# Performance work log

Hardware: AMD Instinct MI355X
Metric: run time of the kernel (lower is better)

## Reference

```python
import jax, jax.numpy as jnp
import numpy as np

NSTEP, NGRID = 365, 50000
PRECS = 1e-05
# [lo, hi] physical ranges for the first 12 HBV parameters (routing params unused, routOpt=False)
PARA_RANGES = np.array([
    [1, 6], [50, 1000], [0.05, 0.9], [0.01, 0.5], [0.001, 0.2], [0.2, 1],
    [0, 10], [0, 100], [-2.5, 2.5], [0.5, 10], [0, 0.1], [0, 0.2],
], dtype=np.float32)


def setup_inputs() -> dict:
    key = jax.random.key(0)
    k1, k2 = jax.random.split(key)
    x = jax.random.uniform(k1, (NSTEP, NGRID, 3), dtype=jnp.float32)
    parameters = jax.random.uniform(k2, (NGRID, 14), dtype=jnp.float32)
    return {"x": x, "parameters": parameters}


def _hbv_forward(x, parameters):
    P = x[:, :, 0]       # precip   [Nstep, Ngrid]
    T = x[:, :, 1]       # temp
    ETpot = x[:, :, 2]   # potential ET
    lo = jnp.asarray(PARA_RANGES[:, 0])
    hi = jnp.asarray(PARA_RANGES[:, 1])
    p = lo + parameters[:, :12] * (hi - lo)  # [Ngrid, 12]
    (parBETA, parFC, parK0, parK1, parK2, parLP, parPERC, parUZL,
     parTT, parCFMAX, parCFR, parCWH) = [p[:, i] for i in range(12)]

    ngrid = P.shape[1]
    init = tuple(jnp.full((ngrid,), 0.001, dtype=jnp.float32) for _ in range(5))

    def step(carry, inp):
        SNOWPACK, MELTWATER, SM, SUZ, SLZ = carry
        PRECIP, Tt, ETp = inp
        is_rain = (Tt >= parTT).astype(jnp.float32)
        RAIN = PRECIP * is_rain
        SNOW = PRECIP * (1.0 - is_rain)
        SNOWPACK = SNOWPACK + SNOW
        melt = jnp.minimum(jnp.maximum(parCFMAX * (Tt - parTT), 0.0), SNOWPACK)
        MELTWATER = MELTWATER + melt
        SNOWPACK = SNOWPACK - melt
        refreezing = jnp.minimum(jnp.maximum(parCFR * parCFMAX * (parTT - Tt), 0.0), MELTWATER)
        SNOWPACK = SNOWPACK + refreezing
        MELTWATER = MELTWATER - refreezing
        tosoil = jnp.maximum(MELTWATER - parCWH * SNOWPACK, 0.0)
        MELTWATER = MELTWATER - tosoil
        soil_wetness = jnp.clip((SM / parFC) ** parBETA, 0.0, 1.0)
        recharge = (RAIN + tosoil) * soil_wetness
        SM = SM + RAIN + tosoil - recharge
        excess = jnp.maximum(SM - parFC, 0.0)
        SM = SM - excess
        evapfactor = jnp.clip(SM / (parLP * parFC), 0.0, 1.0)
        ETact = jnp.minimum(SM, ETp * evapfactor)
        SM = jnp.maximum(SM - ETact, PRECS)
        SUZ = SUZ + recharge + excess
        PERC = jnp.minimum(SUZ, parPERC)
        SUZ = SUZ - PERC
        Q0 = parK0 * jnp.maximum(SUZ - parUZL, 0.0)
        SUZ = SUZ - Q0
        Q1 = parK1 * SUZ
        SUZ = SUZ - Q1
        SLZ = SLZ + PERC
        Q2 = parK2 * SLZ
        SLZ = SLZ - Q2
        return (SNOWPACK, MELTWATER, SM, SUZ, SLZ), Q0 + Q1 + Q2

    _, Qsim = jax.lax.scan(step, init, (P, T, ETpot))
    return Qsim[..., None]  # [Nstep, Ngrid, 1]


def reference(x, parameters):
    return _hbv_forward(x, parameters)
```

## Files before the change

### kernel.cpp

```cpp
#include <hip/hip_runtime.h>

#define NSTEP 365
#define NGRID 50000
#define PRECS_F 1e-5f
#define CHUNK 16

#if defined(__has_builtin)
#  if __has_builtin(__builtin_amdgcn_exp2f) && __has_builtin(__builtin_amdgcn_logf)
#    define FAST_EXP2(x) __builtin_amdgcn_exp2f(x)
#    define FAST_LOG2(x) __builtin_amdgcn_logf(x)
#  endif
#endif
#ifndef FAST_EXP2
#  define FAST_EXP2(x) exp2f(x)
#  define FAST_LOG2(x) log2f(x)
#endif

__global__ __launch_bounds__(64) void hbv_kernel(const float* __restrict__ x,
                                                 const float* __restrict__ params,
                                                 float* __restrict__ out) {
    const int g = blockIdx.x * blockDim.x + threadIdx.x;
    if (g >= NGRID) return;

    const float* pr = params + (size_t)g * 14;
    float r0 = pr[0], r1 = pr[1], r2 = pr[2], r3 = pr[3], r4 = pr[4], r5 = pr[5];
    float r6 = pr[6], r7 = pr[7], r8 = pr[8], r9 = pr[9], r10 = pr[10], r11 = pr[11];

    const float parBETA  = 1.0f   + r0  * 5.0f;
    const float parFC    = 50.0f  + r1  * 950.0f;
    const float parK0    = 0.05f  + r2  * 0.85f;
    const float parK1    = 0.01f  + r3  * 0.49f;
    const float parK2    = 0.001f + r4  * 0.199f;
    const float parLP    = 0.2f   + r5  * 0.8f;
    const float parPERC  =          r6  * 10.0f;
    const float parUZL   =          r7  * 100.0f;
    const float parTT    = -2.5f  + r8  * 5.0f;
    const float parCFMAX = 0.5f   + r9  * 9.5f;
    const float parCFR   =          r10 * 0.1f;
    const float parCWH   =          r11 * 0.2f;

    const float invFC     = 1.0f / parFC;
    const float invLPFC   = 1.0f / (parLP * parFC);
    const float cfr_cfmax = parCFR * parCFMAX;

    float SNOWPACK = 0.001f, MELTWATER = 0.001f, SM = 0.001f, SUZ = 0.001f, SLZ = 0.001f;

    const int nchunks = (NSTEP + CHUNK - 1) / CHUNK;

    float AP[CHUNK], AT[CHUNK], AE[CHUNK];
    float BP[CHUNK], BT[CHUNK], BE[CHUNK];

    auto load_chunk = [&](int cidx, float (&P)[CHUNK], float (&T)[CHUNK], float (&E)[CHUNK]) {
        const int tbase = cidx * CHUNK;
        #pragma unroll
        for (int j = 0; j < CHUNK; ++j) {
            int t = tbase + j;
            t = (t < NSTEP) ? t : (NSTEP - 1);
            const float* p = x + ((size_t)t * NGRID + g) * 3;
            P[j] = p[0];
            T[j] = p[1];
            E[j] = p[2];
        }
    };

    auto compute_chunk = [&](int cidx, const float (&P)[CHUNK], const float (&T)[CHUNK],
                             const float (&E)[CHUNK]) {
        const int t0 = cidx * CHUNK;
        #pragma unroll
        for (int j = 0; j < CHUNK; ++j) {
            const float PRECIP = P[j];
            const float Tt     = T[j];
            const float ETp    = E[j];

            float RAIN = (Tt >= parTT) ? PRECIP : 0.0f;
            float SNOW = PRECIP - RAIN;
            SNOWPACK += SNOW;
            float melt = fminf(fmaxf(parCFMAX * (Tt - parTT), 0.0f), SNOWPACK);
            MELTWATER += melt;
            SNOWPACK  -= melt;
            float refreeze = fminf(fmaxf(cfr_cfmax * (parTT - Tt), 0.0f), MELTWATER);
            SNOWPACK  += refreeze;
            MELTWATER -= refreeze;
            float tosoil = fmaxf(MELTWATER - parCWH * SNOWPACK, 0.0f);
            MELTWATER -= tosoil;

            float ratio = SM * invFC;
            float sw = FAST_EXP2(parBETA * FAST_LOG2(ratio));
            sw = fminf(fmaxf(sw, 0.0f), 1.0f);
            float recharge = (RAIN + tosoil) * sw;
            SM += RAIN + tosoil - recharge;
            float excess = fmaxf(SM - parFC, 0.0f);
            SM -= excess;
            float evapfactor = fminf(fmaxf(SM * invLPFC, 0.0f), 1.0f);
            float ETact = fminf(SM, ETp * evapfactor);
            SM = fmaxf(SM - ETact, PRECS_F);

            SUZ += recharge + excess;
            float PERC = fminf(SUZ, parPERC);
            SUZ -= PERC;
            float Q0 = parK0 * fmaxf(SUZ - parUZL, 0.0f);
            SUZ -= Q0;
            float Q1 = parK1 * SUZ;
            SUZ -= Q1;
            SLZ += PERC;
            float Q2 = parK2 * SLZ;
            SLZ -= Q2;

            const int t = t0 + j;
            if (t < NSTEP) out[(size_t)t * NGRID + g] = Q0 + Q1 + Q2;
        }
    };

    load_chunk(0, AP, AT, AE);
    int c = 0;
    for (;;) {
        if (c + 1 < nchunks) load_chunk(c + 1, BP, BT, BE);
        compute_chunk(c, AP, AT, AE);
        if (++c >= nchunks) break;
        if (c + 1 < nchunks) load_chunk(c + 1, AP, AT, AE);
        compute_chunk(c, BP, BT, BE);
        if (++c >= nchunks) break;
    }
}

extern "C" void kernel_launch(void* const* d_in, const int* in_sizes, int n_in,
                              void* d_out, int out_size, void* d_ws, size_t ws_size,
                              hipStream_t stream) {
    const float* x      = (const float*)d_in[0];
    const float* params = (const float*)d_in[1];
    float* out          = (float*)d_out;

    const int block = 64;
    const int grid  = (NGRID + block - 1) / block;
    hbv_kernel<<<grid, block, 0, stream>>>(x, params, out);
}
```

Baseline: 324.3 us.

## Stage input chunks into LDS via async global_load_lds with double buffering

Replaces per-thread register prefetch of strided P/T/E values with coalesced 16-byte direct global-to-LDS loads covering each block's contiguous 192-float row segment per timestep, double-buffered across chunks. Explicit vmcnt waits let the next chunk's loads overlap computation of the current one. This aims to cut load instruction count and improve coalescing and latency hiding. It relies on single-wave blocks for LDS visibility without barriers and on hand-tuned waitcnt values.

```diff
diff --git a/kernel.cpp b/kernel.cpp
--- a/kernel.cpp
+++ b/kernel.cpp
@@ -4,6 +4,10 @@
 #define NGRID 50000
 #define PRECS_F 1e-5f
 #define CHUNK 16
+#define NCHUNKS ((NSTEP + CHUNK - 1) / CHUNK)
+#define ROWDW   (NGRID * 3)
+#define XSIZE   (NSTEP * ROWDW)
+#define LOADS_PER_CHUNK 12
 
 #if defined(__has_builtin)
 #  if __has_builtin(__builtin_amdgcn_exp2f) && __has_builtin(__builtin_amdgcn_logf)
@@ -16,15 +20,23 @@
 #  define FAST_LOG2(x) log2f(x)
 #endif
 
+typedef __attribute__((address_space(3))) void lds_void_t;
+typedef const __attribute__((address_space(1))) void glb_void_t;
+
 __global__ __launch_bounds__(64) void hbv_kernel(const float* __restrict__ x,
                                                  const float* __restrict__ params,
                                                  float* __restrict__ out) {
-    const int g = blockIdx.x * blockDim.x + threadIdx.x;
-    if (g >= NGRID) return;
+    __shared__ float lds[2][CHUNK * 192];
+
+    const int  lane  = threadIdx.x;
+    const int  bid   = blockIdx.x;
+    const int  gidx  = bid * 64 + lane;
+    const int  g     = (gidx < NGRID) ? gidx : (NGRID - 1);
+    const bool valid = (gidx < NGRID);
 
     const float* pr = params + (size_t)g * 14;
-    float r0 = pr[0], r1 = pr[1], r2 = pr[2], r3 = pr[3], r4 = pr[4], r5 = pr[5];
-    float r6 = pr[6], r7 = pr[7], r8 = pr[8], r9 = pr[9], r10 = pr[10], r11 = pr[11];
+    const float r0 = pr[0], r1 = pr[1], r2 = pr[2], r3 = pr[3], r4 = pr[4], r5 = pr[5];
+    const float r6 = pr[6], r7 = pr[7], r8 = pr[8], r9 = pr[9], r10 = pr[10], r11 = pr[11];
 
     const float parBETA  = 1.0f   + r0  * 5.0f;
     const float parFC    = 50.0f  + r1  * 950.0f;
@@ -45,32 +57,31 @@
 
     float SNOWPACK = 0.001f, MELTWATER = 0.001f, SM = 0.001f, SUZ = 0.001f, SLZ = 0.001f;
 
-    const int nchunks = (NSTEP + CHUNK - 1) / CHUNK;
-
-    float AP[CHUNK], AT[CHUNK], AE[CHUNK];
-    float BP[CHUNK], BT[CHUNK], BE[CHUNK];
-
-    auto load_chunk = [&](int cidx, float (&P)[CHUNK], float (&T)[CHUNK], float (&E)[CHUNK]) {
-        const int tbase = cidx * CHUNK;
+    auto stage = [&](int buf, int cidx) {
+        const int t0 = cidx * CHUNK;
         #pragma unroll
-        for (int j = 0; j < CHUNK; ++j) {
-            int t = tbase + j;
+        for (int i = 0; i < LOADS_PER_CHUNK; ++i) {
+            const int group = i * 64 + lane;
+            const int r     = group / 48;
+            const int wg    = group % 48;
+            int t = t0 + r;
             t = (t < NSTEP) ? t : (NSTEP - 1);
-            const float* p = x + ((size_t)t * NGRID + g) * 3;
-            P[j] = p[0];
-            T[j] = p[1];
-            E[j] = p[2];
+            size_t off = (size_t)t * ROWDW + (size_t)bid * 192 + (size_t)(wg * 4);
+            if (off > (size_t)(XSIZE - 4)) off = (size_t)(XSIZE - 4);
+            __builtin_amdgcn_global_load_lds((glb_void_t*)(x + off),
+                                             (lds_void_t*)&lds[buf][i * 256],
+                                             16, 0, 0);
         }
     };
 
-    auto compute_chunk = [&](int cidx, const float (&P)[CHUNK], const float (&T)[CHUNK],
-                             const float (&E)[CHUNK]) {
+    auto compute = [&](int buf, int cidx) {
         const int t0 = cidx * CHUNK;
+        const float* __restrict__ L = &lds[buf][0];
         #pragma unroll
         for (int j = 0; j < CHUNK; ++j) {
-            const float PRECIP = P[j];
-            const float Tt     = T[j];
-            const float ETp    = E[j];
+            const float PRECIP = L[j * 192 + lane * 3 + 0];
+            const float Tt     = L[j * 192 + lane * 3 + 1];
+            const float ETp    = L[j * 192 + lane * 3 + 2];
 
             float RAIN = (Tt >= parTT) ? PRECIP : 0.0f;
             float SNOW = PRECIP - RAIN;
@@ -107,19 +118,20 @@
             SLZ -= Q2;
 
             const int t = t0 + j;
-            if (t < NSTEP) out[(size_t)t * NGRID + g] = Q0 + Q1 + Q2;
+            if (valid && (t < NSTEP)) out[(size_t)t * NGRID + gidx] = Q0 + Q1 + Q2;
         }
     };
 
-    load_chunk(0, AP, AT, AE);
-    int c = 0;
-    for (;;) {
-        if (c + 1 < nchunks) load_chunk(c + 1, BP, BT, BE);
-        compute_chunk(c, AP, AT, AE);
-        if (++c >= nchunks) break;
-        if (c + 1 < nchunks) load_chunk(c + 1, AP, AT, AE);
-        compute_chunk(c, BP, BT, BE);
-        if (++c >= nchunks) break;
+    stage(0, 0);
+    for (int c = 0; c < NCHUNKS; ++c) {
+        if (c + 1 < NCHUNKS) {
+            stage((c + 1) & 1, c + 1);
+            asm volatile("s_waitcnt vmcnt(12)" ::: "memory");
+        } else {
+            asm volatile("s_waitcnt vmcnt(0)" ::: "memory");
+        }
+        __builtin_amdgcn_sched_barrier(0);
+        compute(c & 1, c);
     }
 }
 
```

Measured after the change: 333.7 us. +2.9%, slower.
